# Performance work log

Hardware: AMD Instinct MI355X
Metric: run time of the kernel (lower is better)

Reference implementation:

```python
import jax, jax.numpy as jnp
import numpy as np
import math

H = 8        # n_heads
FACTOR = 5   # ProbSparse factor


def layer_norm(x, g, b, eps=1e-5):
    m = x.mean(-1, keepdims=True)
    v = ((x - m) ** 2).mean(-1, keepdims=True)
    return (x - m) / jnp.sqrt(v + eps) * g + b


def conv1d_circular(x, w, b=None):
    # x: [B, L, Cin], w: [Cout, Cin, 3]; Conv1d(k=3, padding=1, padding_mode='circular')
    xp = jnp.concatenate([x[:, -1:], x, x[:, :1]], axis=1)
    y = jax.lax.conv_general_dilated(xp.transpose(0, 2, 1), w, (1,), 'VALID',
                                     dimension_numbers=('NCH', 'OIH', 'NCH'))
    if b is not None:
        y = y + b[None, :, None]
    return y.transpose(0, 2, 1)


def pos_encoding(L, d):
    pos = jnp.arange(L, dtype=jnp.float32)[:, None]
    div = jnp.exp(jnp.arange(0, d, 2, dtype=jnp.float32) * (-math.log(10000.0) / d))
    pe = jnp.zeros((L, d), dtype=jnp.float32)
    pe = pe.at[:, 0::2].set(jnp.sin(pos * div))
    pe = pe.at[:, 1::2].set(jnp.cos(pos * div))
    return pe


def prob_attention(rng, Q, K, V):
    # Q, K, V: [B, H, L, E]; non-causal ProbSparse self-attention (mask_flag=False)
    B, Hh, L, E = Q.shape
    c = FACTOR * int(np.ceil(np.log(L)))
    U_part = min(c, L)  # sampled keys per query (sparsity measurement)
    u = min(c, L)       # number of active (top) queries
    idx = jax.random.randint(rng, (L, U_part), 0, L)          # shared over B,H as in torch
    K_sample = K[:, :, idx]                                   # [B,H,L,U,E] gather
    QK_sample = jnp.einsum('bhle,bhlue->bhlu', Q, K_sample)
    M = QK_sample.max(-1) - QK_sample.sum(-1) / L             # sparsity score per query
    M_top = jax.lax.top_k(M, u)[1]                            # [B,H,u] active query ids
    Q_red = jnp.take_along_axis(Q, M_top[..., None], axis=2)  # [B,H,u,E]
    scores = jnp.einsum('bhue,bhle->bhul', Q_red, K) * (1.0 / math.sqrt(E))
    attn = jax.nn.softmax(scores, axis=-1)
    upd = jnp.einsum('bhul,bhle->bhue', attn, V)
    # initial context: mean of V for every query; overwrite active queries
    ctx = jnp.broadcast_to(V.mean(axis=2, keepdims=True), (B, Hh, L, E))
    bi = jnp.arange(B)[:, None, None]
    hi = jnp.arange(Hh)[None, :, None]
    ctx = ctx.at[bi, hi, M_top].set(upd)
    return ctx.transpose(0, 2, 1, 3)  # [B,L,H,E]


def encoder_layer(rng, x, Wq, bq, Wk, bk, Wv, bv, Wo, bo, g1, b1, w1, bf1, w2, bf2, g2, b2):
    B, L, D = x.shape
    dh = D // H
    q = (x @ Wq.T + bq).reshape(B, L, H, dh).transpose(0, 2, 1, 3)
    k = (x @ Wk.T + bk).reshape(B, L, H, dh).transpose(0, 2, 1, 3)
    v = (x @ Wv.T + bv).reshape(B, L, H, dh).transpose(0, 2, 1, 3)
    o = prob_attention(rng, q, k, v).reshape(B, L, D)
    x = x + (o @ Wo.T + bo)            # dropout is identity in eval
    x = layer_norm(x, g1, b1)
    y = jax.nn.gelu(x @ w1.T + bf1, approximate=False)  # conv1 k=1 == linear
    y = y @ w2.T + bf2
    return layer_norm(x + y, g2, b2)


def conv_distill(x, w, b, bg, bb):
    # Conv1d(circular,k=3) -> BatchNorm1d(eval: mean 0, var 1) -> ELU -> MaxPool1d(3,2,1)
    y = conv1d_circular(x, w, b)
    y = y / math.sqrt(1.0 + 1e-5) * bg + bb
    y = jax.nn.elu(y)
    yc = jnp.pad(y.transpose(0, 2, 1), ((0, 0), (0, 0), (1, 1)), constant_values=-jnp.inf)
    p = jax.lax.reduce_window(yc, -jnp.inf, jax.lax.max, (1, 1, 3), (1, 1, 2), 'VALID')
    return p.transpose(0, 2, 1)  # [B, L//2, D]


def forward(x_enc, emb_w, Wq, bq, Wk, bk, Wv, bv, Wo, bo, ln1_g, ln1_b, ff_w1, ff_b1, ff_w2, ff_b2, ln2_g, ln2_b, cv_w, cv_b, bn_g, bn_b, norm_g, norm_b):
    B, L, _ = x_enc.shape
    D = emb_w.shape[0]
    x = conv1d_circular(x_enc, emb_w) + pos_encoding(L, D)[None]  # GazeEmbedding
    base = jax.random.key(42)
    EL = Wq.shape[0]
    for i in range(EL):
        rng = jax.random.fold_in(base, i)
        x = encoder_layer(rng, x, Wq[i], bq[i], Wk[i], bk[i], Wv[i], bv[i], Wo[i], bo[i],
                          ln1_g[i], ln1_b[i], ff_w1[i], ff_b1[i], ff_w2[i], ff_b2[i], ln2_g[i], ln2_b[i])
        if i < EL - 1:
            x = conv_distill(x, cv_w[i], cv_b[i], bn_g[i], bn_b[i])
    return layer_norm(x, norm_g, norm_b)


def setup_inputs() -> dict:
    key = jax.random.key(0)
    ks = jax.random.split(key, 16)
    B, L, C, D, F, EL = 4, 2048, 2, 512, 512, 3
    s = 0.02
    return {
        'x_enc': jax.random.normal(ks[0], (B, L, C), jnp.float32),
        'emb_w': jax.random.normal(ks[1], (D, C, 3), jnp.float32) * s,
        'Wq': jax.random.normal(ks[2], (EL, D, D), jnp.float32) * s,
        'bq': jnp.zeros((EL, D), jnp.float32),
        'Wk': jax.random.normal(ks[3], (EL, D, D), jnp.float32) * s,
        'bk': jnp.zeros((EL, D), jnp.float32),
        'Wv': jax.random.normal(ks[4], (EL, D, D), jnp.float32) * s,
        'bv': jnp.zeros((EL, D), jnp.float32),
        'Wo': jax.random.normal(ks[5], (EL, D, D), jnp.float32) * s,
        'bo': jnp.zeros((EL, D), jnp.float32),
        'ln1_g': jnp.ones((EL, D), jnp.float32),
        'ln1_b': jnp.zeros((EL, D), jnp.float32),
        'ff_w1': jax.random.normal(ks[6], (EL, F, D), jnp.float32) * s,
        'ff_b1': jnp.zeros((EL, F), jnp.float32),
        'ff_w2': jax.random.normal(ks[7], (EL, D, F), jnp.float32) * s,
        'ff_b2': jnp.zeros((EL, D), jnp.float32),
        'ln2_g': jnp.ones((EL, D), jnp.float32),
        'ln2_b': jnp.zeros((EL, D), jnp.float32),
        'cv_w': jax.random.normal(ks[8], (EL - 1, D, D, 3), jnp.float32) * s,
        'cv_b': jnp.zeros((EL - 1, D), jnp.float32),
        'bn_g': jnp.ones((EL - 1, D), jnp.float32),
        'bn_b': jnp.zeros((EL - 1, D), jnp.float32),
        'norm_g': jnp.ones((D,), jnp.float32),
        'norm_b': jnp.zeros((D,), jnp.float32),
    }


def reference(x_enc, emb_w, Wq, bq, Wk, bk, Wv, bv, Wo, bo, ln1_g, ln1_b, ff_w1, ff_b1, ff_w2, ff_b2, ln2_g, ln2_b, cv_w, cv_b, bn_g, bn_b, norm_g, norm_b):
    return forward(x_enc, emb_w, Wq, bq, Wk, bk, Wv, bv, Wo, bo, ln1_g, ln1_b, ff_w1, ff_b1, ff_w2, ff_b2, ln2_g, ln2_b, cv_w, cv_b, bn_g, bn_b, norm_g, norm_b)
```

## Files before the change

kernel.cpp:

```cpp
#include <hip/hip_runtime.h>
#include <cmath>
#include <cstdint>

#define D_MODEL 512
#define NH 8
#define DH 64

static inline int ceil_div(int a, int b) { return (a + b - 1) / b; }

typedef __attribute__((ext_vector_type(8))) short short8;
typedef __attribute__((ext_vector_type(4))) float floatx4;

__device__ __forceinline__ unsigned short f2bf(float f) {
  uint32_t u = __float_as_uint(f);
  uint32_t r = (u + 0x7fffu + ((u >> 16) & 1u)) >> 16;
  return (unsigned short)r;
}
__device__ __forceinline__ float bf2f(unsigned short s) {
  return __uint_as_float(((uint32_t)s) << 16);
}

#define TF_ROTL(x, r) (((x) << (r)) | ((x) >> (32 - (r))))

__host__ __device__ inline void threefry2x32(uint32_t k0, uint32_t k1,
                                             uint32_t x0, uint32_t x1,
                                             uint32_t* o0, uint32_t* o1) {
  uint32_t ks2 = k0 ^ k1 ^ 0x1BD11BDAu;
  x0 += k0; x1 += k1;
#define TF_R4(a, b, c, d)                                    \
  x0 += x1; x1 = TF_ROTL(x1, a); x1 ^= x0;                   \
  x0 += x1; x1 = TF_ROTL(x1, b); x1 ^= x0;                   \
  x0 += x1; x1 = TF_ROTL(x1, c); x1 ^= x0;                   \
  x0 += x1; x1 = TF_ROTL(x1, d); x1 ^= x0;
  TF_R4(13, 15, 26, 6);  x0 += k1;  x1 += ks2 + 1u;
  TF_R4(17, 29, 16, 24); x0 += ks2; x1 += k0 + 2u;
  TF_R4(13, 15, 26, 6);  x0 += k0;  x1 += k1 + 3u;
  TF_R4(17, 29, 16, 24); x0 += k1;  x1 += ks2 + 4u;
  TF_R4(13, 15, 26, 6);  x0 += ks2; x1 += k0 + 5u;
#undef TF_R4
  *o0 = x0; *o1 = x1;
}

__global__ __launch_bounds__(256) void cast_bf16_kernel(
    const float* __restrict__ src, unsigned short* __restrict__ dst, int n) {
  int i = (blockIdx.x * 256 + threadIdx.x) * 4;
  if (i >= n) return;
  float4 v = *(const float4*)(src + i);
  ushort4 o;
  o.x = f2bf(v.x); o.y = f2bf(v.y); o.z = f2bf(v.z); o.w = f2bf(v.w);
  *(ushort4*)(dst + i) = o;
}

__global__ __launch_bounds__(256) void cast_seg_kernel(
    const float* __restrict__ src, unsigned short* __restrict__ dst,
    int n_per_layer, int total, int dst_stride, int dst_off) {
  int i = (blockIdx.x * 256 + threadIdx.x) * 4;
  if (i >= total) return;
  int layer = i / n_per_layer, off = i - layer * n_per_layer;
  float4 v = *(const float4*)(src + i);
  ushort4 o;
  o.x = f2bf(v.x); o.y = f2bf(v.y); o.z = f2bf(v.z); o.w = f2bf(v.w);
  *(ushort4*)(dst + (size_t)layer * dst_stride + dst_off + off) = o;
}

__global__ __launch_bounds__(256) void embed_kernel(
    const float* __restrict__ x_enc, const float* __restrict__ emb_w,
    float* __restrict__ x, unsigned short* __restrict__ xb, int B, int L) {
  int i = blockIdx.x * 256 + threadIdx.x;
  int total = B * L * D_MODEL;
  if (i >= total) return;
  int d = i % D_MODEL;
  int l = (i / D_MODEL) % L;
  int b = i / (D_MODEL * L);
  int lm = (l == 0) ? (L - 1) : (l - 1);
  int lp = (l == L - 1) ? 0 : (l + 1);
  const float* w = emb_w + d * 6;
  const float* xb_in = x_enc + (size_t)b * L * 2;
  float acc = 0.f;
  acc += xb_in[lm * 2 + 0] * w[0] + xb_in[l * 2 + 0] * w[1] + xb_in[lp * 2 + 0] * w[2];
  acc += xb_in[lm * 2 + 1] * w[3] + xb_in[l * 2 + 1] * w[4] + xb_in[lp * 2 + 1] * w[5];
  int j = d >> 1;
  const float coef = -0.017988946039015985f;
  float div = expf((float)(2 * j) * coef);
  float ang = (float)l * div;
  float pe = (d & 1) ? cosf(ang) : sinf(ang);
  float v = acc + pe;
  x[i] = v;
  xb[i] = f2bf(v);
}

__global__ __launch_bounds__(256) void ln_kernel(
    const float* __restrict__ in, const float* __restrict__ g,
    const float* __restrict__ b, float* __restrict__ out) {
  int row = blockIdx.x;
  int t = threadIdx.x;
  const float* xr = in + (size_t)row * D_MODEL;
  float v0 = xr[t], v1 = xr[t + 256];
  __shared__ float red[256];
  red[t] = v0 + v1;
  __syncthreads();
  for (int s = 128; s > 0; s >>= 1) { if (t < s) red[t] += red[t + s]; __syncthreads(); }
  float mean = red[0] * (1.0f / 512.0f);
  __syncthreads();
  float d0 = v0 - mean, d1 = v1 - mean;
  red[t] = d0 * d0 + d1 * d1;
  __syncthreads();
  for (int s = 128; s > 0; s >>= 1) { if (t < s) red[t] += red[t + s]; __syncthreads(); }
  float var = red[0] * (1.0f / 512.0f);
  float rstd = 1.0f / sqrtf(var + 1e-5f);
  float* outr = out + (size_t)row * D_MODEL;
  outr[t]       = d0 * rstd * g[t]       + b[t];
  outr[t + 256] = d1 * rstd * g[t + 256] + b[t + 256];
}

__global__ __launch_bounds__(256) void ln_dual_kernel(
    const float* __restrict__ in, const float* __restrict__ g,
    const float* __restrict__ b, float* __restrict__ out,
    unsigned short* __restrict__ out16) {
  int row = blockIdx.x;
  int t = threadIdx.x;
  const float* xr = in + (size_t)row * D_MODEL;
  float v0 = xr[t], v1 = xr[t + 256];
  __shared__ float red[256];
  red[t] = v0 + v1;
  __syncthreads();
  for (int s = 128; s > 0; s >>= 1) { if (t < s) red[t] += red[t + s]; __syncthreads(); }
  float mean = red[0] * (1.0f / 512.0f);
  __syncthreads();
  float d0 = v0 - mean, d1 = v1 - mean;
  red[t] = d0 * d0 + d1 * d1;
  __syncthreads();
  for (int s = 128; s > 0; s >>= 1) { if (t < s) red[t] += red[t + s]; __syncthreads(); }
  float var = red[0] * (1.0f / 512.0f);
  float rstd = 1.0f / sqrtf(var + 1e-5f);
  float* outr = out + (size_t)row * D_MODEL;
  unsigned short* o16 = out16 + (size_t)row * D_MODEL;
  float r0 = d0 * rstd * g[t] + b[t];
  float r1 = d1 * rstd * g[t + 256] + b[t + 256];
  outr[t] = r0;       o16[t] = f2bf(r0);
  outr[t + 256] = r1; o16[t + 256] = f2bf(r1);
}

__device__ __forceinline__ float epilogue_apply(int MODE, float v, float r,
                                                float g, float bb, float scl) {
  if (MODE == 1) {
    v = 0.5f * v * (1.0f + erff(v * 0.7071067811865475f));
  } else if (MODE == 2) {
    v += r;
  } else if (MODE == 3) {
    v = v * scl * g + bb;
    v = (v > 0.f) ? v : expm1f(v);
  }
  return v;
}


__device__ __forceinline__ void gload16(const void* g, void* l) {
  __builtin_amdgcn_global_load_lds(
      (const __attribute__((address_space(1))) unsigned int*)g,
      (__attribute__((address_space(3))) unsigned int*)l, 16, 0, 0);
}

__device__ __forceinline__ int xcd_swz(int orig, int nwg) {
  int q = nwg >> 3, r = nwg & 7;
  int x = orig & 7, o = orig >> 3;
  return (x < r ? x * (q + 1) : r * (q + 1) + (x - r) * q) + o;
}

__device__ __forceinline__ void stage64(const unsigned short* __restrict__ G,
                                        int ldk, int row0, int k0,
                                        unsigned short* lds, int tid) {
  const int wave = tid >> 6;
#pragma unroll
  for (int iss = 0; iss < 2; ++iss) {
    int s = iss * 256 + tid;
    int r = s >> 3;
    int cs = (s & 7) ^ (r & 7);
    gload16(G + (size_t)(row0 + r) * ldk + k0 + cs * 8,
            lds + (size_t)(iss * 256 + wave * 64) * 8);
  }
}

__device__ __forceinline__ short8 frag64(const unsigned short* t, int row,
                                         int chunk) {
  return *(const short8*)(t + row * 64 + ((chunk ^ (row & 7)) * 8));
}

struct Acc4 { floatx4 v[2][2]; };

__device__ __forceinline__ void gemm64_core(
    const unsigned short* __restrict__ A, int lda,
    const unsigned short* __restrict__ Bt, int ldb, int K, int bm, int bn,
    unsigned short* lds , int tid, Acc4& out) {
  const int wave = tid >> 6, lane = tid & 63;
  const int wm = (wave >> 1) * 32, wn = (wave & 1) * 32;
  const int quad = lane >> 4, l16 = lane & 15;
  floatx4 z = {0.f, 0.f, 0.f, 0.f};
  floatx4 a00 = z, a01 = z, a10 = z, a11 = z;
  stage64(A, lda, bm, 0, lds, tid);
  stage64(Bt, ldb, bn, 0, lds + 4096, tid);
  __syncthreads();
  const int nk = K >> 6;
  for (int t = 0; t < nk; ++t) {
    const int cur = (t & 1) * 8192;
    if (t + 1 < nk) {
      const int nxt = 8192 - cur;
      stage64(A, lda, bm, (t + 1) << 6, lds + nxt, tid);
      stage64(Bt, ldb, bn, (t + 1) << 6, lds + nxt + 4096, tid);
    }
    const unsigned short* At = lds + cur;
    const unsigned short* Bl = lds + cur + 4096;
#pragma unroll
    for (int ks = 0; ks < 2; ++ks) {
      short8 f0 = frag64(At, wm + l16,      ks * 4 + quad);
      short8 f1 = frag64(At, wm + 16 + l16, ks * 4 + quad);
      short8 g0 = frag64(Bl, wn + l16,      ks * 4 + quad);
      short8 g1 = frag64(Bl, wn + 16 + l16, ks * 4 + quad);
      a00 = __builtin_amdgcn_mfma_f32_16x16x32_bf16(f0, g0, a00, 0, 0, 0);
      a01 = __builtin_amdgcn_mfma_f32_16x16x32_bf16(f0, g1, a01, 0, 0, 0);
      a10 = __builtin_amdgcn_mfma_f32_16x16x32_bf16(f1, g0, a10, 0, 0, 0);
      a11 = __builtin_amdgcn_mfma_f32_16x16x32_bf16(f1, g1, a11, 0, 0, 0);
    }
    __syncthreads();
  }
  out.v[0][0] = a00; out.v[0][1] = a01; out.v[1][0] = a10; out.v[1][1] = a11;
}

template <int MODE, int OUT>
__global__ __launch_bounds__(256) void bgemm_kernel(
    const unsigned short* __restrict__ A, const unsigned short* __restrict__ Bt,
    const float* __restrict__ bias, const float* __restrict__ R,
    const float* __restrict__ gvec, const float* __restrict__ bvec,
    float* __restrict__ C, unsigned short* __restrict__ C16,
    int M, int N, int K, float scl) {
  __shared__ unsigned short lds[16384];
  const int tid = threadIdx.x;
  const int gridN = N >> 6;
  const int wgid = xcd_swz(blockIdx.x, (int)gridDim.x);
  const int bn = (wgid % gridN) * 64;
  const int bm = (wgid / gridN) * 64;
  Acc4 acc;
  gemm64_core(A, K, Bt, K, K, bm, bn, lds, tid, acc);
  const int wave = tid >> 6, lane = tid & 63;
  const int wm = (wave >> 1) * 32, wn = (wave & 1) * 32;
  const int quad = lane >> 4, l16 = lane & 15;
#pragma unroll
  for (int i = 0; i < 2; ++i) {
#pragma unroll
    for (int j = 0; j < 2; ++j) {
      int col = bn + wn + j * 16 + l16;
#pragma unroll
      for (int p = 0; p < 4; ++p) {
        int row = bm + wm + i * 16 + quad * 4 + p;
        float v = acc.v[i][j][p] + bias[col];
        v = epilogue_apply(MODE, v, (MODE == 2) ? R[(size_t)row * N + col] : 0.f,
                           (MODE == 3) ? gvec[col] : 0.f,
                           (MODE == 3) ? bvec[col] : 0.f, scl);
        if (OUT & 1) C[(size_t)row * N + col] = v;
        if (OUT & 2) C16[(size_t)row * N + col] = f2bf(v);
      }
    }
  }
}

template <int MODE, int OUT>
static void run_bgemm(const unsigned short* A, const unsigned short* Bt,
                      const float* bias, const float* R, const float* g,
                      const float* bb, float* C, unsigned short* C16,
                      int M, int N, int K, float scl, hipStream_t stream) {
  int nwg = (N / 64) * (M / 64);
  bgemm_kernel<MODE, OUT><<<nwg, 256, 0, stream>>>(A, Bt, bias, R, g, bb, C,
                                                   C16, M, N, K, scl);
}

__global__ __launch_bounds__(256) void qkv_gemm_kernel(
    const unsigned short* __restrict__ A, const unsigned short* __restrict__ Bt,
    const float* __restrict__ bqp, const float* __restrict__ bkp,
    const float* __restrict__ bvp, float* __restrict__ Cq,
    float* __restrict__ Cv, unsigned short* __restrict__ K16o, int M, int K) {
  __shared__ unsigned short lds[16384];
  const int tid = threadIdx.x;
  const int gridN = 24;
  const int wgid = xcd_swz(blockIdx.x, (int)gridDim.x);
  const int bn = (wgid % gridN) * 64;
  const int bm = (wgid / gridN) * 64;
  Acc4 acc;
  gemm64_core(A, K, Bt, K, K, bm, bn, lds, tid, acc);
  const int wave = tid >> 6, lane = tid & 63;
  const int wm = (wave >> 1) * 32, wn = (wave & 1) * 32;
  const int quad = lane >> 4, l16 = lane & 15;
#pragma unroll
  for (int i = 0; i < 2; ++i) {
#pragma unroll
    for (int j = 0; j < 2; ++j) {
      int col = bn + wn + j * 16 + l16;
      int seg = col >> 9, nn = col & 511;
      const float* bp = (seg == 0) ? bqp : (seg == 1) ? bkp : bvp;
      float bsv = bp[nn];
#pragma unroll
      for (int p = 0; p < 4; ++p) {
        int row = bm + wm + i * 16 + quad * 4 + p;
        float v = acc.v[i][j][p] + bsv;
        if (seg == 1) {
          K16o[(size_t)row * 512 + nn] = f2bf(v);
        } else {
          float* Cd = (seg == 0) ? Cq : Cv;
          Cd[(size_t)row * 512 + nn] = v;
        }
      }
    }
  }
}

__global__ __launch_bounds__(256) void sparse_qk_fused_kernel(
    const float* __restrict__ Q, const unsigned short* __restrict__ K16,
    float* __restrict__ Mout, int B, int L, int U, uint32_t k0, uint32_t k1) {
  __shared__ int idxl[64];
  __shared__ float wmax[4][8];
  __shared__ float wsum[4][8];
  int bl = blockIdx.x;
  int b = bl / L, l = bl - b * L;
  int tid = threadIdx.x;
  int wave = tid >> 6, lane = tid & 63;
  if (tid < U) {
    uint32_t o0, o1;
    threefry2x32(k0, k1, 0u, (uint32_t)(l * U + tid), &o0, &o1);
    idxl[tid] = (int)((o0 ^ o1) & (uint32_t)(L - 1));
  }
  int h = lane >> 3;
  const float4* qr = (const float4*)(Q + (size_t)bl * D_MODEL + lane * 8);
  float4 q0 = qr[0], q1 = qr[1];
  float qv[8] = {q0.x, q0.y, q0.z, q0.w, q1.x, q1.y, q1.z, q1.w};
  __syncthreads();
  float mx = -INFINITY, sm = 0.f;
  for (int u = wave; u < U; u += 4) {
    int ki = idxl[u];
    short8 k8 = *(const short8*)(K16 + ((size_t)b * L + ki) * D_MODEL + lane * 8);
    float p = 0.f;
#pragma unroll
    for (int e = 0; e < 8; ++e) p += qv[e] * bf2f((unsigned short)k8[e]);
    p += __shfl_xor(p, 1);
    p += __shfl_xor(p, 2);
    p += __shfl_xor(p, 4);
    mx = fmaxf(mx, p);
    sm += p;
  }
  if ((lane & 7) == 0) { wmax[wave][h] = mx; wsum[wave][h] = sm; }
  __syncthreads();
  if (tid < 8) {
    float m = fmaxf(fmaxf(wmax[0][tid], wmax[1][tid]),
                    fmaxf(wmax[2][tid], wmax[3][tid]));
    float s = wsum[0][tid] + wsum[1][tid] + wsum[2][tid] + wsum[3][tid];
    Mout[((size_t)(b * NH + tid)) * L + l] = m - s / (float)L;
  }
}

template <int NE>
__global__ __launch_bounds__(256) void topk_kernel(
    const float* __restrict__ Mv, int* __restrict__ Mtop,
    unsigned int* __restrict__ bmap, int words, int u) {
  int bh = blockIdx.x;
  int t = threadIdx.x;
  int wave = t >> 6, lane = t & 63;
  const int base = wave * 64 * NE;
  float vals[NE];
  const float* src = Mv + (size_t)bh * (NE * 256);
#pragma unroll
  for (int i = 0; i < NE; ++i) vals[i] = src[base + i * 64 + lane];
  if (t < words) bmap[bh * words + t] = 0u;
  __shared__ float cv[4][40];
  __shared__ int ci[4][40];
  for (int it = 0; it < u; ++it) {
    float bv = -INFINITY;
    int bi = 0x7fffffff;
#pragma unroll
    for (int i = 0; i < NE; ++i) {
      float v = vals[i];
      int ix = base + i * 64 + lane;
      if (v > bv || (v == bv && ix < bi)) { bv = v; bi = ix; }
    }
#pragma unroll
    for (int k = 32; k; k >>= 1) {
      float ov = __shfl_xor(bv, k);
      int oi = __shfl_xor(bi, k);
      if (ov > bv || (ov == bv && oi < bi)) { bv = ov; bi = oi; }
    }
    if (lane == 0) { cv[wave][it] = bv; ci[wave][it] = bi; }
#pragma unroll
    for (int i = 0; i < NE; ++i)
      if (bi == base + i * 64 + lane) vals[i] = -INFINITY;
  }
  __syncthreads();
  if (t < 4 * u) {
    int w = t / u, p = t - w * u;
    float mv = cv[w][p];
    int mi = ci[w][p];
    int rank = p;
    for (int w2 = 0; w2 < 4; ++w2) {
      if (w2 == w) continue;
      int lo = 0, hi = u;
      while (lo < hi) {
        int mid = (lo + hi) >> 1;
        float v2 = cv[w2][mid];
        int i2 = ci[w2][mid];
        if (v2 > mv || (v2 == mv && i2 < mi)) lo = mid + 1;
        else hi = mid;
      }
      rank += lo;
    }
    if (rank < u) {
      Mtop[bh * u + rank] = mi;
      atomicOr(&bmap[bh * words + (mi >> 5)], 1u << (mi & 31));
    }
  }
}

static void run_topk(const float* Mv, int* Mtop, unsigned int* bmap, int L,
                     int u, hipStream_t stream) {
  int words = L / 32;
  if (L == 2048)      topk_kernel<8><<<32, 256, 0, stream>>>(Mv, Mtop, bmap, words, u);
  else if (L == 1024) topk_kernel<4><<<32, 256, 0, stream>>>(Mv, Mtop, bmap, words, u);
  else                topk_kernel<2><<<32, 256, 0, stream>>>(Mv, Mtop, bmap, words, u);
}

__global__ void vmean_zero_kernel(float* __restrict__ vmean) {
  vmean[blockIdx.x * 256 + threadIdx.x] = 0.f;
}

__global__ __launch_bounds__(256) void vmean_partial_kernel(
    const float* __restrict__ V, float* __restrict__ vmean, int L) {
  int b = blockIdx.y;
  int chunk = blockIdx.x;
  int rows = L >> 6;
  int t = threadIdx.x;
  const float* base = V + ((size_t)b * L + (size_t)chunk * rows) * D_MODEL;
  float s0 = 0.f, s1 = 0.f;
  for (int r = 0; r < rows; ++r) {
    s0 += base[(size_t)r * D_MODEL + t];
    s1 += base[(size_t)r * D_MODEL + t + 256];
  }
  float invL = 1.0f / (float)L;
  atomicAdd(&vmean[b * D_MODEL + t], s0 * invL);
  atomicAdd(&vmean[b * D_MODEL + t + 256], s1 * invL);
}

__global__ void fill_ctx_kernel(const float* __restrict__ vmean,
                                const unsigned int* __restrict__ bmap,
                                float* __restrict__ O, int B, int L,
                                int words) {
  int i = blockIdx.x * 256 + threadIdx.x;
  int total = B * L * D_MODEL;
  if (i >= total) return;
  int dcol = i % D_MODEL;
  int l = (i / D_MODEL) % L;
  int b = i / (D_MODEL * L);
  int h = dcol >> 6;
  unsigned int w = bmap[(b * NH + h) * words + (l >> 5)];
  O[i] = ((w >> (l & 31)) & 1u) ? 0.f : vmean[b * D_MODEL + dcol];
}

__global__ void pack_qred_kernel(const float* __restrict__ Q,
                                 const int* __restrict__ Mtop,
                                 unsigned short* __restrict__ qred, int L,
                                 int U) {
  int z = blockIdx.x;
  int b = z / NH, h = z % NH;
  int t = threadIdx.x;
  int d = t & 63;
  for (int r = t >> 6; r < 64; r += 4) {
    float v = 0.f;
    if (r < U) {
      int l = Mtop[z * U + r];
      v = Q[((size_t)(b * L + l)) * D_MODEL + h * DH + d];
    }
    qred[((size_t)z * 64 + r) * 64 + d] = f2bf(v);
  }
}

__global__ __launch_bounds__(256) void scores_mfma_kernel(
    const unsigned short* __restrict__ qred16,
    const unsigned short* __restrict__ k16, float* __restrict__ S, int L) {
  __shared__ unsigned short lds[16384];
  const int z = blockIdx.y;
  const int b = z >> 3, h = z & 7;
  const int bn = blockIdx.x * 64;
  const int tid = threadIdx.x;
  Acc4 acc;
  gemm64_core(qred16 + (size_t)z * 4096, 64,
              k16 + (size_t)b * L * D_MODEL + h * DH, D_MODEL, 64, 0, bn, lds,
              tid, acc);
  float* Sz = S + (size_t)z * 64 * L;
  const int wave = tid >> 6, lane = tid & 63;
  const int wm = (wave >> 1) * 32, wn = (wave & 1) * 32;
  const int quad = lane >> 4, l16 = lane & 15;
#pragma unroll
  for (int i = 0; i < 2; ++i) {
#pragma unroll
    for (int j = 0; j < 2; ++j) {
      int col = bn + wn + j * 16 + l16;
#pragma unroll
      for (int p = 0; p < 4; ++p) {
        int row = wm + i * 16 + quad * 4 + p;
        Sz[(size_t)row * L + col] = 0.125f * acc.v[i][j][p];
      }
    }
  }
}

template <int LC>
__global__ __launch_bounds__(256) void softmax_kernel(float* __restrict__ S,
                                                      int U) {
  constexpr int NE = LC / 256;
  int rid = blockIdx.x;
  int z = rid / U, r = rid % U;
  float* row = S + (size_t)z * 64 * LC + (size_t)r * LC;
  int t = threadIdx.x;
  float vals[NE];
  float m = -INFINITY;
#pragma unroll
  for (int i = 0; i < NE; ++i) {
    vals[i] = row[t + i * 256];
    m = fmaxf(m, vals[i]);
  }
  __shared__ float red[256];
  red[t] = m;
  __syncthreads();
  for (int s = 128; s > 0; s >>= 1) { if (t < s) red[t] = fmaxf(red[t], red[t + s]); __syncthreads(); }
  m = red[0];
  __syncthreads();
  float sum = 0.f;
#pragma unroll
  for (int i = 0; i < NE; ++i) {
    vals[i] = expf(vals[i] - m);
    sum += vals[i];
  }
  red[t] = sum;
  __syncthreads();
  for (int s = 128; s > 0; s >>= 1) { if (t < s) red[t] += red[t + s]; __syncthreads(); }
  float inv = 1.0f / red[0];
#pragma unroll
  for (int i = 0; i < NE; ++i) row[t + i * 256] = vals[i] * inv;
}

static void run_softmax(float* S, int L, int U, hipStream_t stream) {
  int blocks = 32 * U;
  if (L == 2048)      softmax_kernel<2048><<<blocks, 256, 0, stream>>>(S, U);
  else if (L == 1024) softmax_kernel<1024><<<blocks, 256, 0, stream>>>(S, U);
  else                softmax_kernel<512><<<blocks, 256, 0, stream>>>(S, U);
}

#define PV_LC 128

template <int U>
__global__ __launch_bounds__(256) void pv_kernel(
    const float* __restrict__ P, const float* __restrict__ V,
    const int* __restrict__ Mtop, float* __restrict__ O, int L) {
  __shared__ float Pl[U][PV_LC];
  __shared__ float Vl[PV_LC][DH + 4];
  const int z = blockIdx.y;
  const int b = z / NH, h = z % NH;
  const int c0 = blockIdx.x * PV_LC;
  const int tid = threadIdx.x;
  const float* Pz = P + (size_t)z * 64 * L + c0;
  for (int i4 = tid; i4 < U * (PV_LC / 4); i4 += 256) {
    int r = i4 / (PV_LC / 4);
    int lq = (i4 % (PV_LC / 4)) * 4;
    float4 p4 = *(const float4*)(Pz + (size_t)r * L + lq);
    Pl[r][lq + 0] = p4.x; Pl[r][lq + 1] = p4.y;
    Pl[r][lq + 2] = p4.z; Pl[r][lq + 3] = p4.w;
  }
  const float* Vb = V + ((size_t)b * L + c0) * D_MODEL + h * DH;
  for (int i4 = tid; i4 < PV_LC * (DH / 4); i4 += 256) {
    int l = i4 >> 4;
    int d4 = (i4 & 15) * 4;
    float4 v4 = *(const float4*)(Vb + (size_t)l * D_MODEL + d4);
    Vl[l][d4 + 0] = v4.x; Vl[l][d4 + 1] = v4.y;
    Vl[l][d4 + 2] = v4.z; Vl[l][d4 + 3] = v4.w;
  }
  __syncthreads();
  const int wave = tid >> 6, lane = tid & 63;
  constexpr int NJ = (U + 3) / 4;
  float acc[NJ] = {};
  for (int l = 0; l < PV_LC; ++l) {
    float vv = Vl[l][lane];
#pragma unroll
    for (int j = 0; j < NJ; ++j) {
      int r = wave + 4 * j;
      if (r < U) acc[j] += Pl[r][l] * vv;
    }
  }
#pragma unroll
  for (int j = 0; j < NJ; ++j) {
    int r = wave + 4 * j;
    if (r < U) {
      int ml = Mtop[z * U + r];
      atomicAdd(&O[((size_t)(b * L + ml)) * D_MODEL + h * DH + lane], acc[j]);
    }
  }
}

static void run_pv(const float* P, const float* V, const int* Mtop, float* O,
                   int L, int U, hipStream_t stream) {
  dim3 gg(L / PV_LC, 32);
  if (U == 40)      pv_kernel<40><<<gg, 256, 0, stream>>>(P, V, Mtop, O, L);
  else if (U == 35) pv_kernel<35><<<gg, 256, 0, stream>>>(P, V, Mtop, O, L);
  else              pv_kernel<64><<<gg, 256, 0, stream>>>(P, V, Mtop, O, L);
}

__global__ void im2col_kernel(const float* __restrict__ X,
                              unsigned short* __restrict__ Y, int B, int L) {
  int i = blockIdx.x * 256 + threadIdx.x;
  int total = B * L * 1536;
  if (i >= total) return;
  int ck = i % 1536;
  int l = (i / 1536) % L;
  int b = i / (1536 * L);
  int c = ck / 3, k = ck % 3;
  int lm = l + k - 1;
  if (lm < 0) lm += L;
  else if (lm >= L) lm -= L;
  Y[i] = f2bf(X[((size_t)(b * L + lm)) * D_MODEL + c]);
}

__global__ void maxpool_kernel(const float* __restrict__ Y,
                               float* __restrict__ X,
                               unsigned short* __restrict__ Xb, int B, int L) {
  int Lo = L / 2;
  int i = blockIdx.x * 256 + threadIdx.x;
  int total = B * Lo * D_MODEL;
  if (i >= total) return;
  int d = i % D_MODEL;
  int lp = (i / D_MODEL) % Lo;
  int b = i / (D_MODEL * Lo);
  int l0 = 2 * lp - 1;
  float m = -INFINITY;
#pragma unroll
  for (int k = 0; k < 3; ++k) {
    int l = l0 + k;
    if (l >= 0 && l < L) m = fmaxf(m, Y[((size_t)(b * L + l)) * D_MODEL + d]);
  }
  X[i] = m;
  Xb[i] = f2bf(m);
}

extern "C" void kernel_launch(void* const* d_in, const int* in_sizes, int n_in,
                              void* d_out, int out_size, void* d_ws,
                              size_t ws_size, hipStream_t stream) {
  const float* x_enc  = (const float*)d_in[0];
  const float* emb_w  = (const float*)d_in[1];
  const float* Wq     = (const float*)d_in[2];
  const float* bq     = (const float*)d_in[3];
  const float* Wk     = (const float*)d_in[4];
  const float* bk     = (const float*)d_in[5];
  const float* Wv     = (const float*)d_in[6];
  const float* bv     = (const float*)d_in[7];
  const float* Wo     = (const float*)d_in[8];
  const float* bo     = (const float*)d_in[9];
  const float* ln1_g  = (const float*)d_in[10];
  const float* ln1_b  = (const float*)d_in[11];
  const float* ff_w1  = (const float*)d_in[12];
  const float* ff_b1  = (const float*)d_in[13];
  const float* ff_w2  = (const float*)d_in[14];
  const float* ff_b2  = (const float*)d_in[15];
  const float* ln2_g  = (const float*)d_in[16];
  const float* ln2_b  = (const float*)d_in[17];
  const float* cv_w   = (const float*)d_in[18];
  const float* cv_b   = (const float*)d_in[19];
  const float* bn_g   = (const float*)d_in[20];
  const float* bn_b   = (const float*)d_in[21];
  const float* norm_g = (const float*)d_in[22];
  const float* norm_b = (const float*)d_in[23];

  const int B = 4, L0 = 2048, EL = 3;
  const size_t SZ = (size_t)B * 2048 * 512;
  float* ws   = (float*)d_ws;
  float* xbuf = ws;
  float* ebuf = ws + SZ;
  float* qbuf = ws + 2 * SZ;
  float* kbuf = ws + 3 * SZ;
  float* vbuf = ws + 4 * SZ;
  float* obuf = ws + 5 * SZ;
  float* sm   = ws + 6 * SZ;
  float*         d_M     = sm;
  int*           d_Mtop  = (int*)(sm + 65536);
  float*         d_vmean = sm + 65536 + 1280;
  unsigned int*  d_bmap  = (unsigned int*)(sm + 65536 + 1280 + 2048);
  unsigned short* qred16 = (unsigned short*)(sm + 65536 + 1280 + 2048 + 2048);
  unsigned short* wgt  = (unsigned short*)(ws + 6 * SZ + 160000);
  unsigned short* qkvw = wgt;
  unsigned short* wow  = wgt + 3 * 786432;
  unsigned short* w1w  = wow + 3 * 262144;
  unsigned short* w2w  = w1w + 3 * 262144;
  unsigned short* cvw  = w2w + 3 * 262144;

  float* Sbuf = ebuf;
  const float inv_s = 1.0f / sqrtf(1.0f + 1e-5f);

  {
    int g3 = 786432 / 4 / 256;
    cast_seg_kernel<<<g3, 256, 0, stream>>>(Wq, qkvw, 262144, 786432, 786432, 0);
    cast_seg_kernel<<<g3, 256, 0, stream>>>(Wk, qkvw, 262144, 786432, 786432, 262144);
    cast_seg_kernel<<<g3, 256, 0, stream>>>(Wv, qkvw, 262144, 786432, 786432, 524288);
    cast_seg_kernel<<<g3, 256, 0, stream>>>(Wo, wow, 262144, 786432, 262144, 0);
    cast_seg_kernel<<<g3, 256, 0, stream>>>(ff_w1, w1w, 262144, 786432, 262144, 0);
    cast_seg_kernel<<<g3, 256, 0, stream>>>(ff_w2, w2w, 262144, 786432, 262144, 0);
    cast_seg_kernel<<<1536, 256, 0, stream>>>(cv_w, cvw, 786432, 1572864, 786432, 0);
  }

  embed_kernel<<<ceil_div(B * L0 * D_MODEL, 256), 256, 0, stream>>>(
      x_enc, emb_w, xbuf, (unsigned short*)ebuf, B, L0);
  unsigned short* xb16 = (unsigned short*)ebuf;

  int L = L0;
  for (int i = 0; i < EL; ++i) {
    const int M_ = B * L;
    int c = 5 * (int)ceil(log((double)L));
    int U = c < L ? c : L;
    int words = L / 32;
    unsigned short* k16 = (unsigned short*)kbuf;

    qkv_gemm_kernel<<<24 * (M_ / 64), 256, 0, stream>>>(
        xb16, qkvw + (size_t)i * 786432, bq + i * 512, bk + i * 512,
        bv + i * 512, qbuf, vbuf, k16, M_, 512);

    uint32_t lk0, lk1, k20, k21;
    threefry2x32(0u, 42u, 0u, (uint32_t)i, &lk0, &lk1);
    threefry2x32(lk0, lk1, 0u, 1u, &k20, &k21);

    sparse_qk_fused_kernel<<<B * L, 256, 0, stream>>>(qbuf, k16, d_M, B, L, U,
                                                      k20, k21);
    run_topk(d_M, d_Mtop, d_bmap, L, U, stream);
    vmean_zero_kernel<<<8, 256, 0, stream>>>(d_vmean);
    vmean_partial_kernel<<<dim3(64, B), 256, 0, stream>>>(vbuf, d_vmean, L);
    fill_ctx_kernel<<<ceil_div(B * L * D_MODEL, 256), 256, 0, stream>>>(
        d_vmean, d_bmap, obuf, B, L, words);

    pack_qred_kernel<<<B * NH, 256, 0, stream>>>(qbuf, d_Mtop, qred16, L, U);
    scores_mfma_kernel<<<dim3(L / 64, B * NH), 256, 0, stream>>>(qred16, k16,
                                                                 Sbuf, L);
    run_softmax(Sbuf, L, U, stream);
    run_pv(Sbuf, vbuf, d_Mtop, obuf, L, U, stream);

    unsigned short* ab16 = (unsigned short*)qbuf;
    cast_bf16_kernel<<<ceil_div(M_ * 512 / 4, 256), 256, 0, stream>>>(
        obuf, ab16, M_ * 512);
    run_bgemm<2, 1>(ab16, wow + (size_t)i * 262144, bo + i * 512, xbuf,
                    nullptr, nullptr, ebuf, nullptr, M_, 512, 512, 0.f,
                    stream);
    ln_dual_kernel<<<M_, 256, 0, stream>>>(ebuf, ln1_g + i * 512,
                                           ln1_b + i * 512, xbuf, ab16);

    unsigned short* ff1b16 = (unsigned short*)obuf;
    run_bgemm<1, 2>(ab16, w1w + (size_t)i * 262144, ff_b1 + i * 512, nullptr,
                    nullptr, nullptr, nullptr, ff1b16, M_, 512, 512, 0.f,
                    stream);
    run_bgemm<2, 1>(ff1b16, w2w + (size_t)i * 262144, ff_b2 + i * 512, xbuf,
                    nullptr, nullptr, ebuf, nullptr, M_, 512, 512, 0.f,
                    stream);
    ln_kernel<<<M_, 256, 0, stream>>>(ebuf, ln2_g + i * 512, ln2_b + i * 512,
                                      xbuf);

    if (i < EL - 1) {
      unsigned short* imb16 = (unsigned short*)qbuf;
      im2col_kernel<<<ceil_div(B * L * 1536, 256), 256, 0, stream>>>(xbuf,
                                                                     imb16, B,
                                                                     L);
      run_bgemm<3, 1>(imb16, cvw + (size_t)i * 786432, cv_b + i * 512, nullptr,
                      bn_g + i * 512, bn_b + i * 512, ebuf, nullptr, M_, 512,
                      1536, inv_s, stream);
      xb16 = (unsigned short*)vbuf + 6291456;
      maxpool_kernel<<<ceil_div(B * (L / 2) * D_MODEL, 256), 256, 0, stream>>>(
          ebuf, xbuf, xb16, B, L);
      L /= 2;
    }
  }

  ln_kernel<<<B * L, 256, 0, stream>>>(xbuf, norm_g, norm_b, (float*)d_out);
}
```

Measured before the change: 785.1 us.

## Fuse im2col into conv GEMM and fold small attention kernels together

Replaces the im2col kernel plus generic GEMM for the distilling conv with a dedicated implicit-GEMM kernel. It reads the bf16 LayerNorm output with circular row offsets, using a weight layout permuted at cast time. The bf16 attention output is now produced directly: fill_ctx writes bf16 and only selected rows are recast after PV. This removes the full-tensor cast. The qred packing and vmean zeroing move into the top-k kernel, and the weight casts are merged into three launches. This cuts launches and removes large intermediate buffers, but adds index arithmetic and relies on power-of-two L.

```diff
diff --git a/kernel.cpp b/kernel.cpp
--- a/kernel.cpp
+++ b/kernel.cpp
@@ -41,26 +41,38 @@
   *o0 = x0; *o1 = x1;
 }
 
-__global__ __launch_bounds__(256) void cast_bf16_kernel(
-    const float* __restrict__ src, unsigned short* __restrict__ dst, int n) {
-  int i = (blockIdx.x * 256 + threadIdx.x) * 4;
-  if (i >= n) return;
-  float4 v = *(const float4*)(src + i);
+__global__ __launch_bounds__(256) void cast3_qkv_kernel(
+    const float* __restrict__ s0, const float* __restrict__ s1,
+    const float* __restrict__ s2, unsigned short* __restrict__ dst) {
+  int sel = blockIdx.x / 768, bb = blockIdx.x % 768;
+  int i = (bb * 256 + threadIdx.x) * 4;
+  const float* s = (sel == 0) ? s0 : (sel == 1) ? s1 : s2;
+  float4 v = *(const float4*)(s + i);
   ushort4 o;
   o.x = f2bf(v.x); o.y = f2bf(v.y); o.z = f2bf(v.z); o.w = f2bf(v.w);
-  *(ushort4*)(dst + i) = o;
-}
-
-__global__ __launch_bounds__(256) void cast_seg_kernel(
-    const float* __restrict__ src, unsigned short* __restrict__ dst,
-    int n_per_layer, int total, int dst_stride, int dst_off) {
-  int i = (blockIdx.x * 256 + threadIdx.x) * 4;
-  if (i >= total) return;
-  int layer = i / n_per_layer, off = i - layer * n_per_layer;
-  float4 v = *(const float4*)(src + i);
+  int layer = i >> 18, off = i & 262143;
+  *(ushort4*)(dst + (size_t)layer * 786432 + sel * 262144 + off) = o;
+}
+
+__global__ __launch_bounds__(256) void cast3_flat_kernel(
+    const float* __restrict__ s0, const float* __restrict__ s1,
+    const float* __restrict__ s2, unsigned short* __restrict__ dst) {
+  int sel = blockIdx.x / 768, bb = blockIdx.x % 768;
+  int i = (bb * 256 + threadIdx.x) * 4;
+  const float* s = (sel == 0) ? s0 : (sel == 1) ? s1 : s2;
+  float4 v = *(const float4*)(s + i);
   ushort4 o;
   o.x = f2bf(v.x); o.y = f2bf(v.y); o.z = f2bf(v.z); o.w = f2bf(v.w);
-  *(ushort4*)(dst + (size_t)layer * dst_stride + dst_off + off) = o;
+  *(ushort4*)(dst + (size_t)sel * 786432 + i) = o;
+}
+
+__global__ __launch_bounds__(256) void cast_cvperm_kernel(
+    const float* __restrict__ src, unsigned short* __restrict__ dst) {
+  int o = blockIdx.x * 256 + threadIdx.x;
+  int m = o / 786432, rem = o % 786432;
+  int n = rem / 1536, q = rem % 1536;
+  int k = q >> 9, c = q & 511;
+  dst[o] = f2bf(src[(size_t)m * 786432 + n * 1536 + c * 3 + k]);
 }
 
 __global__ __launch_bounds__(256) void embed_kernel(
@@ -312,6 +324,82 @@
   }
 }
 
+__global__ __launch_bounds__(256) void conv_gemm_kernel(
+    const unsigned short* __restrict__ Axl, const unsigned short* __restrict__ Bt,
+    const float* __restrict__ bias, const float* __restrict__ gvec,
+    const float* __restrict__ bvec, float* __restrict__ C,
+    int M, int L, int log2L, float scl) {
+  __shared__ unsigned short lds[16384];
+  const int tid = threadIdx.x;
+  const int wgid = xcd_swz(blockIdx.x, (int)gridDim.x);
+  const int bn = (wgid & 7) * 64;
+  const int bm = (wgid >> 3) * 64;
+  const int wave = tid >> 6, lane = tid & 63;
+  const int wm = (wave >> 1) * 32, wn = (wave & 1) * 32;
+  const int quad = lane >> 4, l16 = lane & 15;
+  floatx4 z = {0.f, 0.f, 0.f, 0.f};
+  floatx4 a00 = z, a01 = z, a10 = z, a11 = z;
+
+#define STAGE_A_CONV(T, DST)                                               \
+  {                                                                        \
+    _Pragma("unroll") for (int iss = 0; iss < 2; ++iss) {                  \
+      int s = iss * 256 + tid;                                             \
+      int r = s >> 3;                                                      \
+      int cs = (s & 7) ^ (r & 7);                                          \
+      int row = bm + r;                                                    \
+      int li = row & (L - 1);                                              \
+      int bb2 = row >> log2L;                                              \
+      int l2 = (li + ((T) >> 3) - 1 + L) & (L - 1);                        \
+      gload16(Axl + (((size_t)((bb2 << log2L) + l2)) << 9) +               \
+                  (((T) & 7) << 6) + cs * 8,                               \
+              (DST) + (size_t)(iss * 256 + wave * 64) * 8);                \
+    }                                                                      \
+  }
+
+  STAGE_A_CONV(0, lds);
+  stage64(Bt, 1536, bn, 0, lds + 4096, tid);
+  __syncthreads();
+  for (int t = 0; t < 24; ++t) {
+    const int cur = (t & 1) * 8192;
+    if (t + 1 < 24) {
+      const int nxt = 8192 - cur;
+      STAGE_A_CONV(t + 1, lds + nxt);
+      stage64(Bt, 1536, bn, (t + 1) << 6, lds + nxt + 4096, tid);
+    }
+    const unsigned short* At = lds + cur;
+    const unsigned short* Bl = lds + cur + 4096;
+#pragma unroll
+    for (int ks = 0; ks < 2; ++ks) {
+      short8 f0 = frag64(At, wm + l16,      ks * 4 + quad);
+      short8 f1 = frag64(At, wm + 16 + l16, ks * 4 + quad);
+      short8 g0 = frag64(Bl, wn + l16,      ks * 4 + quad);
+      short8 g1 = frag64(Bl, wn + 16 + l16, ks * 4 + quad);
+      a00 = __builtin_amdgcn_mfma_f32_16x16x32_bf16(f0, g0, a00, 0, 0, 0);
+      a01 = __builtin_amdgcn_mfma_f32_16x16x32_bf16(f0, g1, a01, 0, 0, 0);
+      a10 = __builtin_amdgcn_mfma_f32_16x16x32_bf16(f1, g0, a10, 0, 0, 0);
+      a11 = __builtin_amdgcn_mfma_f32_16x16x32_bf16(f1, g1, a11, 0, 0, 0);
+    }
+    __syncthreads();
+  }
+#undef STAGE_A_CONV
+  floatx4 accs[2][2] = {{a00, a01}, {a10, a11}};
+#pragma unroll
+  for (int i = 0; i < 2; ++i) {
+#pragma unroll
+    for (int j = 0; j < 2; ++j) {
+      int col = bn + wn + j * 16 + l16;
+      float gv = gvec[col], bbv = bvec[col], bsv = bias[col];
+#pragma unroll
+      for (int p = 0; p < 4; ++p) {
+        int row = bm + wm + i * 16 + quad * 4 + p;
+        float v = accs[i][j][p] + bsv;
+        v = epilogue_apply(3, v, 0.f, gv, bbv, scl);
+        C[(size_t)row * 512 + col] = v;
+      }
+    }
+  }
+}
+
 __global__ __launch_bounds__(256) void sparse_qk_fused_kernel(
     const float* __restrict__ Q, const unsigned short* __restrict__ K16,
     float* __restrict__ Mout, int B, int L, int U, uint32_t k0, uint32_t k1) {
@@ -357,9 +445,12 @@
 
 template <int NE>
 __global__ __launch_bounds__(256) void topk_kernel(
-    const float* __restrict__ Mv, int* __restrict__ Mtop,
-    unsigned int* __restrict__ bmap, int words, int u) {
+    const float* __restrict__ Mv, const float* __restrict__ Q,
+    int* __restrict__ Mtop, unsigned int* __restrict__ bmap,
+    unsigned short* __restrict__ qred16, float* __restrict__ vmean,
+    int words, int u, int L) {
   int bh = blockIdx.x;
+  int b = bh >> 3, h = bh & 7;
   int t = threadIdx.x;
   int wave = t >> 6, lane = t & 63;
   const int base = wave * 64 * NE;
@@ -368,8 +459,10 @@
 #pragma unroll
   for (int i = 0; i < NE; ++i) vals[i] = src[base + i * 64 + lane];
   if (t < words) bmap[bh * words + t] = 0u;
+  if (t < 64) vmean[bh * 64 + t] = 0.f;
   __shared__ float cv[4][40];
   __shared__ int ci[4][40];
+  __shared__ int smTop[40];
   for (int it = 0; it < u; ++it) {
     float bv = -INFINITY;
     int bi = 0x7fffffff;
@@ -410,21 +503,32 @@
     }
     if (rank < u) {
       Mtop[bh * u + rank] = mi;
+      smTop[rank] = mi;
       atomicOr(&bmap[bh * words + (mi >> 5)], 1u << (mi & 31));
     }
   }
-}
-
-static void run_topk(const float* Mv, int* Mtop, unsigned int* bmap, int L,
-                     int u, hipStream_t stream) {
+  __syncthreads();
+  int d = t & 63;
+  for (int r = t >> 6; r < 64; r += 4) {
+    float v = 0.f;
+    if (r < u) {
+      int l = smTop[r];
+      v = Q[((size_t)(b * L + l)) * D_MODEL + h * DH + d];
+    }
+    qred16[((size_t)bh * 64 + r) * 64 + d] = f2bf(v);
+  }
+}
+
+static void run_topk(const float* Mv, const float* Q, int* Mtop,
+                     unsigned int* bmap, unsigned short* qred16, float* vmean,
+                     int L, int u, hipStream_t stream) {
   int words = L / 32;
-  if (L == 2048)      topk_kernel<8><<<32, 256, 0, stream>>>(Mv, Mtop, bmap, words, u);
-  else if (L == 1024) topk_kernel<4><<<32, 256, 0, stream>>>(Mv, Mtop, bmap, words, u);
-  else                topk_kernel<2><<<32, 256, 0, stream>>>(Mv, Mtop, bmap, words, u);
-}
-
-__global__ void vmean_zero_kernel(float* __restrict__ vmean) {
-  vmean[blockIdx.x * 256 + threadIdx.x] = 0.f;
+  if (L == 2048)
+    topk_kernel<8><<<32, 256, 0, stream>>>(Mv, Q, Mtop, bmap, qred16, vmean, words, u, L);
+  else if (L == 1024)
+    topk_kernel<4><<<32, 256, 0, stream>>>(Mv, Q, Mtop, bmap, qred16, vmean, words, u, L);
+  else
+    topk_kernel<2><<<32, 256, 0, stream>>>(Mv, Q, Mtop, bmap, qred16, vmean, words, u, L);
 }
 
 __global__ __launch_bounds__(256) void vmean_partial_kernel(
@@ -446,7 +550,8 @@
 
 __global__ void fill_ctx_kernel(const float* __restrict__ vmean,
                                 const unsigned int* __restrict__ bmap,
-                                float* __restrict__ O, int B, int L,
+                                unsigned short* __restrict__ O16,
+                                float* __restrict__ O32, int B, int L,
                                 int words) {
   int i = blockIdx.x * 256 + threadIdx.x;
   int total = B * L * D_MODEL;
@@ -456,24 +561,23 @@
   int b = i / (D_MODEL * L);
   int h = dcol >> 6;
   unsigned int w = bmap[(b * NH + h) * words + (l >> 5)];
-  O[i] = ((w >> (l & 31)) & 1u) ? 0.f : vmean[b * D_MODEL + dcol];
-}
-
-__global__ void pack_qred_kernel(const float* __restrict__ Q,
-                                 const int* __restrict__ Mtop,
-                                 unsigned short* __restrict__ qred, int L,
-                                 int U) {
+  bool sel = (w >> (l & 31)) & 1u;
+  O16[i] = f2bf(sel ? 0.f : vmean[b * D_MODEL + dcol]);
+  if (sel) O32[i] = 0.f;
+}
+
+__global__ void cast_sel_kernel(const float* __restrict__ O32,
+                                const int* __restrict__ Mtop,
+                                unsigned short* __restrict__ O16, int L,
+                                int U) {
   int z = blockIdx.x;
-  int b = z / NH, h = z % NH;
+  int b = z >> 3, h = z & 7;
   int t = threadIdx.x;
   int d = t & 63;
-  for (int r = t >> 6; r < 64; r += 4) {
-    float v = 0.f;
-    if (r < U) {
-      int l = Mtop[z * U + r];
-      v = Q[((size_t)(b * L + l)) * D_MODEL + h * DH + d];
-    }
-    qred[((size_t)z * 64 + r) * 64 + d] = f2bf(v);
+  for (int r = t >> 6; r < U; r += 4) {
+    int l = Mtop[z * U + r];
+    size_t off = ((size_t)(b * L + l)) * D_MODEL + h * DH + d;
+    O16[off] = f2bf(O32[off]);
   }
 }
 
@@ -605,21 +709,6 @@
   if (U == 40)      pv_kernel<40><<<gg, 256, 0, stream>>>(P, V, Mtop, O, L);
   else if (U == 35) pv_kernel<35><<<gg, 256, 0, stream>>>(P, V, Mtop, O, L);
   else              pv_kernel<64><<<gg, 256, 0, stream>>>(P, V, Mtop, O, L);
-}
-
-__global__ void im2col_kernel(const float* __restrict__ X,
-                              unsigned short* __restrict__ Y, int B, int L) {
-  int i = blockIdx.x * 256 + threadIdx.x;
-  int total = B * L * 1536;
-  if (i >= total) return;
-  int ck = i % 1536;
-  int l = (i / 1536) % L;
-  int b = i / (1536 * L);
-  int c = ck / 3, k = ck % 3;
-  int lm = l + k - 1;
-  if (lm < 0) lm += L;
-  else if (lm >= L) lm -= L;
-  Y[i] = f2bf(X[((size_t)(b * L + lm)) * D_MODEL + c]);
 }
 
 __global__ void maxpool_kernel(const float* __restrict__ Y,
@@ -688,30 +777,25 @@
   unsigned short* qred16 = (unsigned short*)(sm + 65536 + 1280 + 2048 + 2048);
   unsigned short* wgt  = (unsigned short*)(ws + 6 * SZ + 160000);
   unsigned short* qkvw = wgt;
-  unsigned short* wow  = wgt + 3 * 786432;
-  unsigned short* w1w  = wow + 3 * 262144;
-  unsigned short* w2w  = w1w + 3 * 262144;
-  unsigned short* cvw  = w2w + 3 * 262144;
+  unsigned short* wof  = wgt + 3 * 786432;
+  unsigned short* wow  = wof;
+  unsigned short* w1w  = wof + 786432;
+  unsigned short* w2w  = wof + 2 * 786432;
+  unsigned short* cvw2 = wof + 3 * 786432;
 
   float* Sbuf = ebuf;
   const float inv_s = 1.0f / sqrtf(1.0f + 1e-5f);
 
-  {
-    int g3 = 786432 / 4 / 256;
-    cast_seg_kernel<<<g3, 256, 0, stream>>>(Wq, qkvw, 262144, 786432, 786432, 0);
-    cast_seg_kernel<<<g3, 256, 0, stream>>>(Wk, qkvw, 262144, 786432, 786432, 262144);
-    cast_seg_kernel<<<g3, 256, 0, stream>>>(Wv, qkvw, 262144, 786432, 786432, 524288);
-    cast_seg_kernel<<<g3, 256, 0, stream>>>(Wo, wow, 262144, 786432, 262144, 0);
-    cast_seg_kernel<<<g3, 256, 0, stream>>>(ff_w1, w1w, 262144, 786432, 262144, 0);
-    cast_seg_kernel<<<g3, 256, 0, stream>>>(ff_w2, w2w, 262144, 786432, 262144, 0);
-    cast_seg_kernel<<<1536, 256, 0, stream>>>(cv_w, cvw, 786432, 1572864, 786432, 0);
-  }
+  cast3_qkv_kernel<<<3 * 768, 256, 0, stream>>>(Wq, Wk, Wv, qkvw);
+  cast3_flat_kernel<<<3 * 768, 256, 0, stream>>>(Wo, ff_w1, ff_w2, wof);
+  cast_cvperm_kernel<<<6144, 256, 0, stream>>>(cv_w, cvw2);
 
   embed_kernel<<<ceil_div(B * L0 * D_MODEL, 256), 256, 0, stream>>>(
       x_enc, emb_w, xbuf, (unsigned short*)ebuf, B, L0);
   unsigned short* xb16 = (unsigned short*)ebuf;
 
   int L = L0;
+  int log2L = 11;
   for (int i = 0; i < EL; ++i) {
     const int M_ = B * L;
     int c = 5 * (int)ceil(log((double)L));
@@ -729,21 +813,18 @@
 
     sparse_qk_fused_kernel<<<B * L, 256, 0, stream>>>(qbuf, k16, d_M, B, L, U,
                                                       k20, k21);
-    run_topk(d_M, d_Mtop, d_bmap, L, U, stream);
-    vmean_zero_kernel<<<8, 256, 0, stream>>>(d_vmean);
+    run_topk(d_M, qbuf, d_Mtop, d_bmap, qred16, d_vmean, L, U, stream);
     vmean_partial_kernel<<<dim3(64, B), 256, 0, stream>>>(vbuf, d_vmean, L);
+    unsigned short* ab16 = (unsigned short*)qbuf;
     fill_ctx_kernel<<<ceil_div(B * L * D_MODEL, 256), 256, 0, stream>>>(
-        d_vmean, d_bmap, obuf, B, L, words);
-
-    pack_qred_kernel<<<B * NH, 256, 0, stream>>>(qbuf, d_Mtop, qred16, L, U);
+        d_vmean, d_bmap, ab16, obuf, B, L, words);
+
     scores_mfma_kernel<<<dim3(L / 64, B * NH), 256, 0, stream>>>(qred16, k16,
                                                                  Sbuf, L);
     run_softmax(Sbuf, L, U, stream);
     run_pv(Sbuf, vbuf, d_Mtop, obuf, L, U, stream);
-
-    unsigned short* ab16 = (unsigned short*)qbuf;
-    cast_bf16_kernel<<<ceil_div(M_ * 512 / 4, 256), 256, 0, stream>>>(
-        obuf, ab16, M_ * 512);
+    cast_sel_kernel<<<B * NH, 256, 0, stream>>>(obuf, d_Mtop, ab16, L, U);
+
     run_bgemm<2, 1>(ab16, wow + (size_t)i * 262144, bo + i * 512, xbuf,
                     nullptr, nullptr, ebuf, nullptr, M_, 512, 512, 0.f,
                     stream);
@@ -757,21 +838,22 @@
     run_bgemm<2, 1>(ff1b16, w2w + (size_t)i * 262144, ff_b2 + i * 512, xbuf,
                     nullptr, nullptr, ebuf, nullptr, M_, 512, 512, 0.f,
                     stream);
-    ln_kernel<<<M_, 256, 0, stream>>>(ebuf, ln2_g + i * 512, ln2_b + i * 512,
-                                      xbuf);
 
     if (i < EL - 1) {
-      unsigned short* imb16 = (unsigned short*)qbuf;
-      im2col_kernel<<<ceil_div(B * L * 1536, 256), 256, 0, stream>>>(xbuf,
-                                                                     imb16, B,
-                                                                     L);
-      run_bgemm<3, 1>(imb16, cvw + (size_t)i * 786432, cv_b + i * 512, nullptr,
-                      bn_g + i * 512, bn_b + i * 512, ebuf, nullptr, M_, 512,
-                      1536, inv_s, stream);
+      unsigned short* xln16 = (unsigned short*)qbuf;
+      ln_dual_kernel<<<M_, 256, 0, stream>>>(ebuf, ln2_g + i * 512,
+                                             ln2_b + i * 512, xbuf, xln16);
+      conv_gemm_kernel<<<8 * (M_ / 64), 256, 0, stream>>>(
+          xln16, cvw2 + (size_t)i * 786432, cv_b + i * 512, bn_g + i * 512,
+          bn_b + i * 512, ebuf, M_, L, log2L, inv_s);
       xb16 = (unsigned short*)vbuf + 6291456;
       maxpool_kernel<<<ceil_div(B * (L / 2) * D_MODEL, 256), 256, 0, stream>>>(
           ebuf, xbuf, xb16, B, L);
       L /= 2;
+      log2L -= 1;
+    } else {
+      ln_kernel<<<M_, 256, 0, stream>>>(ebuf, ln2_g + i * 512,
+                                        ln2_b + i * 512, xbuf);
     }
   }
 
```

New measurement: 741.5 us. 1.06x faster.
